# Performance work log

Hardware: AMD Instinct MI355X
Metric: run time of the kernel (lower is better)

Reference implementation:

```python
import jax, jax.numpy as jnp
import numpy as np

N_TOKEN = 8192
N_EMBED = 512
N_SAMPLE = 10
TAU = 1.0
RHO = 1.0


def setup_inputs() -> dict:
    key = jax.random.key(0)
    k1, k2 = jax.random.split(key)
    inputs = jax.random.normal(k1, (4, 2048, N_EMBED), dtype=jnp.float32)
    embeds = jax.random.normal(k2, (N_TOKEN, N_EMBED), dtype=jnp.float32)
    return {"inputs": inputs, "embeds": embeds}


def reference(inputs, embeds):
    size = inputs.shape
    x = inputs.reshape(-1, N_EMBED)  # (N, D)
    n = x.shape[0]
    # squared distances, scaled by n_token (as in get_distances)
    dists = (jnp.sum(x * x, axis=-1, keepdims=True)
             + jnp.sum(embeds * embeds, axis=-1)[None, :]
             - 2.0 * jnp.matmul(x, embeds.T)) / N_TOKEN  # (N, K)
    logits = -dists / TAU  # categorical(softmax(logits)) == categorical(logits)
    skey = jax.random.fold_in(jax.random.key(0), 1)
    # multinomial with replacement: n_sample i.i.d. categorical draws per row
    samples = jax.random.categorical(skey, logits[:, None, :], axis=-1,
                                     shape=(n, N_SAMPLE))  # (N, n_sample) int
    quantized_embs = embeds[samples].mean(axis=1)  # (N, D) gather + mean
    quantized = x + jax.lax.stop_gradient(quantized_embs - x)  # straight-through
    gkey = jax.random.fold_in(jax.random.key(0), 2)
    gates = jax.random.bernoulli(gkey, RHO, (n,)).astype(x.dtype)[:, None]
    quantized = quantized * gates + (1.0 - gates) * x
    quantized = quantized.reshape(size)
    samples = samples.reshape(size[:-1] + (N_SAMPLE,))
    return quantized, samples
```

## Files before the change

### kernel.cpp

```cpp
#include <hip/hip_runtime.h>
#include <stdint.h>
#include <math.h>

#define N_ROWS 8192
#define N_TOK  8192
#define N_DIM  512
#define N_SAMP 10
#define GK     1536

typedef __attribute__((ext_vector_type(8))) short bf16x8_t;
typedef __attribute__((ext_vector_type(4))) float f32x4_t;

__host__ __device__ __forceinline__ void tf2x32(uint32_t ks0, uint32_t ks1,
                                                uint32_t& x0, uint32_t& x1) {
  uint32_t ks2 = ks0 ^ ks1 ^ 0x1BD11BDAu;
  x0 += ks0; x1 += ks1;
#define TF_ROUND(r) { x0 += x1; x1 = __builtin_rotateleft32(x1, r); x1 ^= x0; }
  TF_ROUND(13) TF_ROUND(15) TF_ROUND(26) TF_ROUND(6)
  x0 += ks1; x1 += ks2 + 1u;
  TF_ROUND(17) TF_ROUND(29) TF_ROUND(16) TF_ROUND(24)
  x0 += ks2; x1 += ks0 + 2u;
  TF_ROUND(13) TF_ROUND(15) TF_ROUND(26) TF_ROUND(6)
  x0 += ks0; x1 += ks1 + 3u;
  TF_ROUND(17) TF_ROUND(29) TF_ROUND(16) TF_ROUND(24)
  x0 += ks1; x1 += ks2 + 4u;
  TF_ROUND(13) TF_ROUND(15) TF_ROUND(26) TF_ROUND(6)
  x0 += ks2; x1 += ks0 + 5u;
#undef TF_ROUND
}

__device__ __forceinline__ unsigned short f2bf_rne(float f) {
  uint32_t u = __float_as_uint(f);
  uint32_t r = (u + 0x7fffu + ((u >> 16) & 1u)) >> 16;
  return (unsigned short)r;
}
__device__ __forceinline__ float bf2f(unsigned short h) {
  return __uint_as_float((uint32_t)h << 16);
}

__device__ __forceinline__ unsigned long long shfl_xor_u64(unsigned long long v, int off) {
  uint32_t lo = (uint32_t)v, hi = (uint32_t)(v >> 32);
  lo = (uint32_t)__shfl_xor((int)lo, off, 64);
  hi = (uint32_t)__shfl_xor((int)hi, off, 64);
  return ((unsigned long long)hi << 32) | lo;
}

__global__ __launch_bounds__(256) void rownorm_kernel(const float* __restrict__ M,
                                                      float* __restrict__ out) {
  int lane = threadIdx.x & 63;
  int row = (int)((blockIdx.x * blockDim.x + threadIdx.x) >> 6);
  const float* p = M + (size_t)row * N_DIM;
  float acc = 0.f;
#pragma unroll
  for (int d = 0; d < N_DIM; d += 64) {
    float v = p[d + lane];
    acc = fmaf(v, v, acc);
  }
#pragma unroll
  for (int off = 32; off; off >>= 1) acc += __shfl_xor(acc, off, 64);
  if (lane == 0) out[row] = acc;
}

__global__ __launch_bounds__(256) void init_champ_kernel(unsigned long long* __restrict__ c) {
  int i = blockIdx.x * 256 + threadIdx.x;
  if (i < N_ROWS * N_SAMP) c[i] = 0xFFFFFFFFFFFFFFFFULL;
}

__global__ __launch_bounds__(256) void init_state_kernel(float* __restrict__ rmin,
                                                         int* __restrict__ ridx) {
  int i = blockIdx.x * 256 + threadIdx.x;
  if (i < N_ROWS * N_SAMP) { rmin[i] = INFINITY; ridx[i] = 0; }
}

__global__ __launch_bounds__(256) void split_kernel(const float* __restrict__ src,
                                                    unsigned short* __restrict__ dst,
                                                    int mode) {
  int t = blockIdx.x * 256 + threadIdx.x;
  int row = t >> 7;
  int c = (t & 127) << 2;
  float4 v = *(const float4*)(src + (size_t)row * N_DIM + c);
  ushort4 hi, lo;
  hi.x = f2bf_rne(v.x); lo.x = f2bf_rne(v.x - bf2f(hi.x));
  hi.y = f2bf_rne(v.y); lo.y = f2bf_rne(v.y - bf2f(hi.y));
  hi.z = f2bf_rne(v.z); lo.z = f2bf_rne(v.z - bf2f(hi.z));
  hi.w = f2bf_rne(v.w); lo.w = f2bf_rne(v.w - bf2f(hi.w));
  unsigned short* base = dst + (size_t)row * GK;
  *(ushort4*)(base + c) = hi;
  if (mode == 0) {
    *(ushort4*)(base + 512 + c) = lo;
    *(ushort4*)(base + 1024 + c) = hi;
  } else {
    *(ushort4*)(base + 512 + c) = hi;
    *(ushort4*)(base + 1024 + c) = lo;
  }
}

__device__ __forceinline__ void async_cp16(const void* g, void* l) {
  __builtin_amdgcn_global_load_lds((const __attribute__((address_space(1))) void*)g,
                                   (__attribute__((address_space(3))) void*)l, 16, 0, 0);
}

__global__ __launch_bounds__(256) void fused_gemm_sample_kernel(
    const unsigned short* __restrict__ A2, const unsigned short* __restrict__ B2,
    const float* __restrict__ xx, const float* __restrict__ ee,
    unsigned long long* __restrict__ champ, uint32_t k0, uint32_t k1) {
  __shared__ __align__(16) unsigned char smem[65536];
  unsigned short* As = (unsigned short*)smem;
  unsigned short* Bs = (unsigned short*)(smem + 16384);
  float* Et = (float*)smem;
  int tid = threadIdx.x;
  int w = tid >> 6, l = tid & 63;

  int bid = blockIdx.y * gridDim.x + blockIdx.x;
  int by = bid & 63;
  int bx = bid >> 6;

  int row0 = by * 128;
  int col0 = bx * 128;
  int wm = (w & 1) * 64, wn = (w >> 1) * 64;
  int quad = l >> 4, r15 = l & 15;

  f32x4_t acc[4][4];
#pragma unroll
  for (int i = 0; i < 4; ++i)
#pragma unroll
    for (int j = 0; j < 4; ++j) acc[i][j] = (f32x4_t){0.f, 0.f, 0.f, 0.f};

  int srow[4], skc[4];
#pragma unroll
  for (int r = 0; r < 4; ++r) {
    int c = tid + 256 * r;
    srow[r] = c >> 3;
    skc[r] = (c & 7) ^ (srow[r] & 7);
  }

  for (int kt = 0; kt < GK; kt += 64) {
#pragma unroll
    for (int r = 0; r < 4; ++r) {
      int c = tid + 256 * r;
      async_cp16(A2 + (size_t)(row0 + srow[r]) * GK + kt + skc[r] * 8, As + c * 8);
      async_cp16(B2 + (size_t)(col0 + srow[r]) * GK + kt + skc[r] * 8, Bs + c * 8);
    }
    __syncthreads();

#pragma unroll
    for (int kk2 = 0; kk2 < 2; ++kk2) {
      bf16x8_t af[4], bf[4];
#pragma unroll
      for (int i = 0; i < 4; ++i) {
        int row = wm + i * 16 + r15;
        int qc = (kk2 * 4 + quad) ^ (r15 & 7);
        af[i] = *(const bf16x8_t*)&As[row * 64 + qc * 8];
      }
#pragma unroll
      for (int j = 0; j < 4; ++j) {
        int row = wn + j * 16 + r15;
        int qc = (kk2 * 4 + quad) ^ (r15 & 7);
        bf[j] = *(const bf16x8_t*)&Bs[row * 64 + qc * 8];
      }
#pragma unroll
      for (int i = 0; i < 4; ++i)
#pragma unroll
        for (int j = 0; j < 4; ++j)
          acc[i][j] = __builtin_amdgcn_mfma_f32_16x16x32_bf16(af[i], bf[j], acc[i][j], 0, 0, 0);
    }
    __syncthreads();
  }

  const float inv_nt = 1.f / 8192.f;
  float eev[4];
#pragma unroll
  for (int j = 0; j < 4; ++j) eev[j] = ee[col0 + wn + j * 16 + r15];
#pragma unroll
  for (int i = 0; i < 4; ++i) {
#pragma unroll
    for (int r = 0; r < 4; ++r) {
      int lrow = wm + i * 16 + quad * 4 + r;
      float xxv = xx[row0 + lrow];
      int mxr = lrow & 31;
#pragma unroll
      for (int j = 0; j < 4; ++j) {
        int col = wn + j * 16 + r15;
        float dist = (xxv + eev[j] - 2.0f * acc[i][j][r]) * inv_nt;
        Et[lrow * 128 + (col ^ mxr)] = expf(dist);
      }
    }
  }
  __syncthreads();

  int lrow = tid >> 1, half = tid & 1;
  int grow = row0 + lrow;
  unsigned long long* cg = champ + (size_t)grow * N_SAMP;
  unsigned long long cw[N_SAMP];
  uint32_t th[N_SAMP];
  int improved = 0;
#pragma unroll
  for (int s = 0; s < N_SAMP; ++s) {
    unsigned long long c = cg[s];
    cw[s] = 0xFFFFFFFFFFFFFFFFULL;
    uint32_t hi = (uint32_t)(c >> 32);
    uint32_t t = 0u;
    if (hi < 0x7F800000u) {
      float ut = expf(-__uint_as_float(hi)) * 0.999999f;
      t = ((uint32_t)(ut * 8388608.0f)) << 9;
    }
    th[s] = t;
  }
  const float tiny = 1.1754943508222875e-38f;
  uint32_t row_c = (uint32_t)grow * 81920u;
  const float* Erow = Et + lrow * 128 + half * 64;
  int mxr = lrow & 31;
  uint32_t kbase = (uint32_t)(col0 + half * 64);

  for (int kk = 0; kk < 64; ++kk) {
    float Ek = Erow[kk ^ mxr];
    uint32_t base_c = row_c + kbase + (uint32_t)kk;
#pragma unroll
    for (int s = 0; s < N_SAMP; ++s) {
      uint32_t x0 = 0u, x1 = base_c + (uint32_t)s * 8192u;
      tf2x32(k0, k1, x0, x1);
      uint32_t bits = x0 ^ x1;
      if (bits >= th[s]) {
        float u = __uint_as_float(0x3f800000u | (bits >> 9)) - 1.0f;
        u = fmaxf(u, tiny);
        float wv = -logf(u) * Ek;
        unsigned long long p = ((unsigned long long)__float_as_uint(wv) << 32)
                             | (kbase + (uint32_t)kk);
        if (p < cw[s]) {
          cw[s] = p;
          float ut = expf(-wv) * 0.999999f;
          uint32_t nt = ((uint32_t)(ut * 8388608.0f)) << 9;
          th[s] = (nt > th[s]) ? nt : th[s];
          improved |= (1 << s);
        }
      }
    }
  }
#pragma unroll
  for (int s = 0; s < N_SAMP; ++s)
    if (improved & (1 << s)) atomicMin(&cg[s], cw[s]);
}

__global__ __launch_bounds__(256) void gemm_nt_kernel(const float* __restrict__ A,
                                                      const float* __restrict__ B,
                                                      const float* __restrict__ xx,
                                                      const float* __restrict__ ee,
                                                      float* __restrict__ E,
                                                      int ks, int KC) {
  __shared__ __align__(16) float Asf[32][68];
  __shared__ __align__(16) float Bsf[32][68];
  int tid = threadIdx.x;
  int row0 = blockIdx.y * 64;
  int colB0 = blockIdx.x * 64 + ks;
  int tx = tid & 15, ty = tid >> 4;
  float acc[4][4] = {};
  for (int d0 = 0; d0 < N_DIM; d0 += 32) {
#pragma unroll
    for (int r = 0; r < 2; ++r) {
      int c = tid + 256 * r;
      int m = c >> 3;
      int dv = (c & 7) << 2;
      const float4 va = *(const float4*)(A + (size_t)(row0 + m) * N_DIM + d0 + dv);
      Asf[dv + 0][m] = va.x; Asf[dv + 1][m] = va.y;
      Asf[dv + 2][m] = va.z; Asf[dv + 3][m] = va.w;
      const float4 vb = *(const float4*)(B + (size_t)(colB0 + m) * N_DIM + d0 + dv);
      Bsf[dv + 0][m] = vb.x; Bsf[dv + 1][m] = vb.y;
      Bsf[dv + 2][m] = vb.z; Bsf[dv + 3][m] = vb.w;
    }
    __syncthreads();
#pragma unroll
    for (int dd = 0; dd < 32; ++dd) {
      float4 a4 = *(const float4*)&Asf[dd][ty << 2];
      float4 b4 = *(const float4*)&Bsf[dd][tx << 2];
      float av[4] = {a4.x, a4.y, a4.z, a4.w};
      float bv[4] = {b4.x, b4.y, b4.z, b4.w};
#pragma unroll
      for (int i = 0; i < 4; ++i)
#pragma unroll
        for (int j = 0; j < 4; ++j)
          acc[i][j] = fmaf(av[i], bv[j], acc[i][j]);
    }
    __syncthreads();
  }
  const float inv_nt = 1.f / 8192.f;
  int colC0 = blockIdx.x * 64;
  float eev[4];
#pragma unroll
  for (int j = 0; j < 4; ++j) eev[j] = ee[ks + colC0 + (tx << 2) + j];
#pragma unroll
  for (int i = 0; i < 4; ++i) {
    int grow = row0 + (ty << 2) + i;
    float xxv = xx[grow];
    float4 v;
    v.x = expf((xxv + eev[0] - 2.0f * acc[i][0]) * inv_nt);
    v.y = expf((xxv + eev[1] - 2.0f * acc[i][1]) * inv_nt);
    v.z = expf((xxv + eev[2] - 2.0f * acc[i][2]) * inv_nt);
    v.w = expf((xxv + eev[3] - 2.0f * acc[i][3]) * inv_nt);
    *(float4*)(E + (size_t)grow * KC + colC0 + (tx << 2)) = v;
  }
}

__global__ __launch_bounds__(256) void sample_kernel(const float* __restrict__ E,
                                                     float* __restrict__ rmin,
                                                     int* __restrict__ ridx,
                                                     int ks, int KC,
                                                     uint32_t k0, uint32_t k1) {
  int lane = threadIdx.x & 63;
  int row = (int)((blockIdx.x * blockDim.x + threadIdx.x) >> 6);
  unsigned long long champ[N_SAMP];
  uint32_t th[N_SAMP];
#pragma unroll
  for (int s = 0; s < N_SAMP; ++s) { champ[s] = 0xFFFFFFFFFFFFFFFFULL; th[s] = 0u; }
  const float tiny = 1.1754943508222875e-38f;
  uint32_t row_c = (uint32_t)row * 81920u;
  const float* Erow = E + (size_t)row * KC;

  float Ek = Erow[lane];
  for (int kk = lane; kk < KC; kk += 64) {
    int nk = (kk + 64 < KC) ? kk + 64 : kk;
    float Ekn = Erow[nk];
    uint32_t k = (uint32_t)(ks + kk);
    uint32_t base_c = row_c + k;
#pragma unroll
    for (int s = 0; s < N_SAMP; ++s) {
      uint32_t x0 = 0u, x1 = base_c + (uint32_t)s * 8192u;
      tf2x32(k0, k1, x0, x1);
      uint32_t bits = x0 ^ x1;
      bool cand = (bits >= th[s]);
      if (__any(cand)) {
        float u = __uint_as_float(0x3f800000u | (bits >> 9)) - 1.0f;
        u = fmaxf(u, tiny);
        float wv = -logf(u) * Ek;
        unsigned long long p = cand
            ? (((unsigned long long)__float_as_uint(wv) << 32) | k)
            : 0xFFFFFFFFFFFFFFFFULL;
#pragma unroll
        for (int off = 1; off < 64; off <<= 1) {
          unsigned long long op = shfl_xor_u64(p, off);
          p = (op < p) ? op : p;
        }
        if (p < champ[s]) {
          champ[s] = p;
          float wmin = __uint_as_float((uint32_t)(p >> 32));
          float ut = expf(-wmin) * 0.999999f;
          th[s] = ((uint32_t)(ut * 8388608.0f)) << 9;
        }
      }
    }
    Ek = Ekn;
  }
#pragma unroll
  for (int s = 0; s < N_SAMP; ++s) {
    if (lane == 0) {
      float v = __uint_as_float((uint32_t)(champ[s] >> 32));
      int id = (int)(uint32_t)(champ[s] & 0xFFFFFFFFu);
      size_t p = (size_t)row * N_SAMP + s;
      if (v < rmin[p]) { rmin[p] = v; ridx[p] = id; }
    }
  }
}

__global__ __launch_bounds__(256) void gather_kernel(const float* __restrict__ emb,
                                                     const unsigned long long* __restrict__ champ,
                                                     const float* __restrict__ x,
                                                     float* __restrict__ outq,
                                                     float* __restrict__ outs) {
  int lane = threadIdx.x & 63;
  int row = (int)((blockIdx.x * blockDim.x + threadIdx.x) >> 6);
  int idx[N_SAMP];
#pragma unroll
  for (int s = 0; s < N_SAMP; ++s)
    idx[s] = (int)(uint32_t)(champ[(size_t)row * N_SAMP + s] & 0xFFFFFFFFu);
  if (lane < N_SAMP) outs[row * N_SAMP + lane] = (float)idx[lane];
#pragma unroll
  for (int h = 0; h < 2; ++h) {
    int c = h * 256 + lane * 4;
    float4 sum = make_float4(0.f, 0.f, 0.f, 0.f);
#pragma unroll
    for (int s = 0; s < N_SAMP; ++s) {
      float4 e = *(const float4*)(emb + (size_t)idx[s] * N_DIM + c);
      sum.x += e.x; sum.y += e.y; sum.z += e.z; sum.w += e.w;
    }
    float4 xv = *(const float4*)(x + (size_t)row * N_DIM + c);
    float4 o;
    o.x = xv.x + (sum.x / 10.0f - xv.x);
    o.y = xv.y + (sum.y / 10.0f - xv.y);
    o.z = xv.z + (sum.z / 10.0f - xv.z);
    o.w = xv.w + (sum.w / 10.0f - xv.w);
    *(float4*)(outq + (size_t)row * N_DIM + c) = o;
  }
}

__global__ __launch_bounds__(256) void gather_fb_kernel(const float* __restrict__ emb,
                                                        const int* __restrict__ ridx,
                                                        const float* __restrict__ x,
                                                        float* __restrict__ outq,
                                                        float* __restrict__ outs) {
  int lane = threadIdx.x & 63;
  int row = (int)((blockIdx.x * blockDim.x + threadIdx.x) >> 6);
  int idx[N_SAMP];
#pragma unroll
  for (int s = 0; s < N_SAMP; ++s) idx[s] = ridx[row * N_SAMP + s];
  if (lane < N_SAMP) outs[row * N_SAMP + lane] = (float)idx[lane];
#pragma unroll
  for (int h = 0; h < 2; ++h) {
    int c = h * 256 + lane * 4;
    float4 sum = make_float4(0.f, 0.f, 0.f, 0.f);
#pragma unroll
    for (int s = 0; s < N_SAMP; ++s) {
      float4 e = *(const float4*)(emb + (size_t)idx[s] * N_DIM + c);
      sum.x += e.x; sum.y += e.y; sum.z += e.z; sum.w += e.w;
    }
    float4 xv = *(const float4*)(x + (size_t)row * N_DIM + c);
    float4 o;
    o.x = xv.x + (sum.x / 10.0f - xv.x);
    o.y = xv.y + (sum.y / 10.0f - xv.y);
    o.z = xv.z + (sum.z / 10.0f - xv.z);
    o.w = xv.w + (sum.w / 10.0f - xv.w);
    *(float4*)(outq + (size_t)row * N_DIM + c) = o;
  }
}

extern "C" void kernel_launch(void* const* d_in, const int* in_sizes, int n_in,
                              void* d_out, int out_size, void* d_ws, size_t ws_size,
                              hipStream_t stream) {
  const float* x = (const float*)d_in[0];
  const float* emb = (const float*)d_in[1];
  float* out_q = (float*)d_out;
  float* out_s = out_q + (size_t)N_ROWS * N_DIM;

  const size_t split_u = (size_t)N_ROWS * GK;
  const size_t fixed_f = (size_t)N_ROWS + N_TOK + 2 * (size_t)N_ROWS * N_SAMP;
  const size_t out_f = (size_t)N_ROWS * N_DIM + (size_t)N_ROWS * N_SAMP;

  uint32_t s0 = 0u, s1 = 1u;
  tf2x32(0u, 0u, s0, s1);

  {
    size_t need = (size_t)(N_ROWS + N_TOK) * 4
                + (size_t)N_ROWS * N_SAMP * 8
                + 2 * split_u * 2;
    if (need <= ws_size) {
      float* xx = (float*)d_ws;
      float* ee = xx + N_ROWS;
      unsigned long long* champ = (unsigned long long*)(ee + N_TOK);
      unsigned short* A2 = (unsigned short*)(champ + (size_t)N_ROWS * N_SAMP);
      unsigned short* B2 = A2 + split_u;

      rownorm_kernel<<<2048, 256, 0, stream>>>(x, xx);
      rownorm_kernel<<<2048, 256, 0, stream>>>(emb, ee);
      init_champ_kernel<<<(N_ROWS * N_SAMP + 255) / 256, 256, 0, stream>>>(champ);
      split_kernel<<<N_ROWS * 128 / 256, 256, 0, stream>>>(x, A2, 0);
      split_kernel<<<N_ROWS * 128 / 256, 256, 0, stream>>>(emb, B2, 1);
      fused_gemm_sample_kernel<<<dim3(64, 64), 256, 0, stream>>>(
          A2, B2, xx, ee, champ, s0, s1);
      gather_kernel<<<2048, 256, 0, stream>>>(emb, champ, x, out_q, out_s);
      return;
    }
  }

  float *xx, *ee, *rmin, *E;
  int* ridx;
  int KC = 0;
  for (int c = 8192; c >= 64; c >>= 1) {
    if ((fixed_f + (size_t)N_ROWS * c) * 4 <= ws_size) { KC = c; break; }
  }
  if (KC) {
    xx = (float*)d_ws;
    ee = xx + N_ROWS;
    rmin = ee + N_TOK;
    ridx = (int*)(rmin + (size_t)N_ROWS * N_SAMP);
    E = (float*)(ridx + (size_t)N_ROWS * N_SAMP);
  } else if (fixed_f * 4 <= ws_size) {
    KC = 512;
    xx = (float*)d_ws;
    ee = xx + N_ROWS;
    rmin = ee + N_TOK;
    ridx = (int*)(rmin + (size_t)N_ROWS * N_SAMP);
    E = out_q;
  } else {
    KC = 256;
    E = out_q;
    float* tail = out_q + (out_f - fixed_f);
    xx = tail;
    ee = xx + N_ROWS;
    rmin = ee + N_TOK;
    ridx = (int*)(rmin + (size_t)N_ROWS * N_SAMP);
  }

  rownorm_kernel<<<2048, 256, 0, stream>>>(x, xx);
  rownorm_kernel<<<2048, 256, 0, stream>>>(emb, ee);
  init_state_kernel<<<(N_ROWS * N_SAMP + 255) / 256, 256, 0, stream>>>(rmin, ridx);
  for (int ks = 0; ks < N_TOK; ks += KC) {
    gemm_nt_kernel<<<dim3(KC / 64, N_ROWS / 64), 256, 0, stream>>>(x, emb, xx, ee, E, ks, KC);
    sample_kernel<<<2048, 256, 0, stream>>>(E, rmin, ridx, ks, KC, s0, s1);
  }
  gather_fb_kernel<<<2048, 256, 0, stream>>>(emb, ridx, x, out_q, out_s);
}
```

Measured before the change: 1.526 ms.

## Halve sampling LDS tile, split epilogue into two passes, outline accept path

The fused GEMM+sampling epilogue now writes the exp-distance tile in two 64-row halves, so LDS shrinks from 64KB to 32KB and launch bounds request 4 blocks per CU. Each row's 128 columns are now handled by four threads instead of two, which shortens the serial Threefry loop per thread. The rare accept path moves into a noinline function that does atomicMin directly instead of keeping per-sample champion registers, cutting register pressure. The cost is an extra barrier round, more global atomics, and a function call on each accepted candidate.

```diff
diff --git a/kernel.cpp b/kernel.cpp
--- a/kernel.cpp
+++ b/kernel.cpp
@@ -43,6 +43,20 @@
   lo = (uint32_t)__shfl_xor((int)lo, off, 64);
   hi = (uint32_t)__shfl_xor((int)hi, off, 64);
   return ((unsigned long long)hi << 32) | lo;
+}
+
+__device__ __attribute__((noinline)) uint32_t accept_publish(
+    uint32_t bits, float Ek, uint32_t kglob, uint32_t th,
+    unsigned long long* __restrict__ cp) {
+  const float tiny = 1.1754943508222875e-38f;
+  float u = __uint_as_float(0x3f800000u | (bits >> 9)) - 1.0f;
+  u = fmaxf(u, tiny);
+  float wv = -logf(u) * Ek;
+  unsigned long long p = ((unsigned long long)__float_as_uint(wv) << 32) | kglob;
+  atomicMin(cp, p);
+  float ut = expf(-wv) * 0.999999f;
+  uint32_t nt = ((uint32_t)(ut * 8388608.0f)) << 9;
+  return (nt > th) ? nt : th;
 }
 
 __global__ __launch_bounds__(256) void rownorm_kernel(const float* __restrict__ M,
@@ -100,11 +114,11 @@
                                    (__attribute__((address_space(3))) void*)l, 16, 0, 0);
 }
 
-__global__ __launch_bounds__(256) void fused_gemm_sample_kernel(
+__global__ __launch_bounds__(256, 4) void fused_gemm_sample_kernel(
     const unsigned short* __restrict__ A2, const unsigned short* __restrict__ B2,
     const float* __restrict__ xx, const float* __restrict__ ee,
     unsigned long long* __restrict__ champ, uint32_t k0, uint32_t k1) {
-  __shared__ __align__(16) unsigned char smem[65536];
+  __shared__ __align__(16) unsigned char smem[32768];
   unsigned short* As = (unsigned short*)smem;
   unsigned short* Bs = (unsigned short*)(smem + 16384);
   float* Et = (float*)smem;
@@ -171,74 +185,65 @@
   float eev[4];
 #pragma unroll
   for (int j = 0; j < 4; ++j) eev[j] = ee[col0 + wn + j * 16 + r15];
-#pragma unroll
-  for (int i = 0; i < 4; ++i) {
-#pragma unroll
-    for (int r = 0; r < 4; ++r) {
-      int lrow = wm + i * 16 + quad * 4 + r;
-      float xxv = xx[row0 + lrow];
-      int mxr = lrow & 31;
-#pragma unroll
-      for (int j = 0; j < 4; ++j) {
-        int col = wn + j * 16 + r15;
-        float dist = (xxv + eev[j] - 2.0f * acc[i][j][r]) * inv_nt;
-        Et[lrow * 128 + (col ^ mxr)] = expf(dist);
-      }
-    }
-  }
-  __syncthreads();
-
-  int lrow = tid >> 1, half = tid & 1;
-  int grow = row0 + lrow;
-  unsigned long long* cg = champ + (size_t)grow * N_SAMP;
-  unsigned long long cw[N_SAMP];
-  uint32_t th[N_SAMP];
-  int improved = 0;
-#pragma unroll
-  for (int s = 0; s < N_SAMP; ++s) {
-    unsigned long long c = cg[s];
-    cw[s] = 0xFFFFFFFFFFFFFFFFULL;
-    uint32_t hi = (uint32_t)(c >> 32);
-    uint32_t t = 0u;
-    if (hi < 0x7F800000u) {
-      float ut = expf(-__uint_as_float(hi)) * 0.999999f;
-      t = ((uint32_t)(ut * 8388608.0f)) << 9;
-    }
-    th[s] = t;
-  }
-  const float tiny = 1.1754943508222875e-38f;
-  uint32_t row_c = (uint32_t)grow * 81920u;
-  const float* Erow = Et + lrow * 128 + half * 64;
-  int mxr = lrow & 31;
-  uint32_t kbase = (uint32_t)(col0 + half * 64);
-
-  for (int kk = 0; kk < 64; ++kk) {
-    float Ek = Erow[kk ^ mxr];
-    uint32_t base_c = row_c + kbase + (uint32_t)kk;
-#pragma unroll
-    for (int s = 0; s < N_SAMP; ++s) {
-      uint32_t x0 = 0u, x1 = base_c + (uint32_t)s * 8192u;
-      tf2x32(k0, k1, x0, x1);
-      uint32_t bits = x0 ^ x1;
-      if (bits >= th[s]) {
-        float u = __uint_as_float(0x3f800000u | (bits >> 9)) - 1.0f;
-        u = fmaxf(u, tiny);
-        float wv = -logf(u) * Ek;
-        unsigned long long p = ((unsigned long long)__float_as_uint(wv) << 32)
-                             | (kbase + (uint32_t)kk);
-        if (p < cw[s]) {
-          cw[s] = p;
-          float ut = expf(-wv) * 0.999999f;
-          uint32_t nt = ((uint32_t)(ut * 8388608.0f)) << 9;
-          th[s] = (nt > th[s]) ? nt : th[s];
-          improved |= (1 << s);
+
+#pragma unroll 1
+  for (int p = 0; p < 2; ++p) {
+    if ((w & 1) == p) {
+#pragma unroll
+      for (int i = 0; i < 4; ++i) {
+#pragma unroll
+        for (int r = 0; r < 4; ++r) {
+          int lr = i * 16 + quad * 4 + r;
+          float xxv = xx[row0 + p * 64 + lr];
+          int mxr = lr & 31;
+#pragma unroll
+          for (int j = 0; j < 4; ++j) {
+            int col = wn + j * 16 + r15;
+            float dist = (xxv + eev[j] - 2.0f * acc[i][j][r]) * inv_nt;
+            Et[lr * 128 + (col ^ mxr)] = expf(dist);
+          }
         }
       }
     }
-  }
-#pragma unroll
-  for (int s = 0; s < N_SAMP; ++s)
-    if (improved & (1 << s)) atomicMin(&cg[s], cw[s]);
+    __syncthreads();
+
+    int lr = tid >> 2;
+    int q4 = tid & 3;
+    int grow = row0 + p * 64 + lr;
+    unsigned long long* cg = champ + (size_t)grow * N_SAMP;
+    uint32_t th[N_SAMP];
+#pragma unroll
+    for (int s = 0; s < N_SAMP; ++s) {
+      unsigned long long c = cg[s];
+      uint32_t hi = (uint32_t)(c >> 32);
+      uint32_t t = 0u;
+      if (hi < 0x7F800000u) {
+        float ut = expf(-__uint_as_float(hi)) * 0.999999f;
+        t = ((uint32_t)(ut * 8388608.0f)) << 9;
+      }
+      th[s] = t;
+    }
+    uint32_t row_c = (uint32_t)grow * 81920u;
+    int mxr = lr & 31;
+    const float* Erow = Et + lr * 128;
+    int colb = q4 * 32;
+
+    for (int c = 0; c < 32; ++c) {
+      int col = colb + c;
+      float Ek = Erow[col ^ mxr];
+      uint32_t kglob = (uint32_t)(col0 + col);
+      uint32_t base_c = row_c + kglob;
+#pragma unroll
+      for (int s = 0; s < N_SAMP; ++s) {
+        uint32_t x0 = 0u, x1 = base_c + (uint32_t)s * 8192u;
+        tf2x32(k0, k1, x0, x1);
+        uint32_t bits = x0 ^ x1;
+        if (bits >= th[s])
+          th[s] = accept_publish(bits, Ek, kglob, th[s], &cg[s]);
+      }
+    }
+    __syncthreads();
+  }
 }
 
 __global__ __launch_bounds__(256) void gemm_nt_kernel(const float* __restrict__ A,
```

Result: slower. 1.881 ms (+23.3%).
